# Performance work log

Measured on AMD Instinct MI355X. Metric: run time of the kernel, lower is better.

The kernel has to match this reference:

```python
import jax, jax.numpy as jnp
import numpy as np

BETA = 0.99      # rootfind_module beta
TOL = 1e-3       # torch loop: while V(fx*a) - t > 0.001
MAX_ITER = 50    # safety cap (torch loop is uncapped but converges)


def _fhat(x, W1, b1, W2, b2):
    # x: (B,1,D) -> (B,1,D)
    h = jnp.tanh(x @ W1 + b1)
    return h @ W2 + b2


def _V_sample(z, Wv1, Wv2):
    # z: (1,D) -> scalar Lyapunov value
    h = jnp.tanh(z @ Wv1)
    y = h @ Wv2
    return jnp.sum(y * y) + 0.01 * jnp.sum(z * z)


def _V(z, Wv1, Wv2):
    # z: (B,1,D) -> (B,1,1)
    h = jnp.tanh(z @ Wv1)
    y = h @ Wv2
    v = jnp.sum(y * y, axis=(-2, -1)) + 0.01 * jnp.sum(z * z, axis=(-2, -1))
    return v[:, None, None]


def _newton_step(fhatx, target, alpha, Wv1, Wv2):
    # newton_iter.forward: F = alpha - (V(fhatx*alpha) - target) / dV/dalpha
    z = fhatx * alpha                                  # (B,1,D)
    Vz = _V(z, Wv1, Wv2)                               # (B,1,1)
    gradV = jax.vmap(jax.grad(_V_sample), in_axes=(0, None, None))(z, Wv1, Wv2)
    dV_da = jnp.sum(gradV * fhatx, axis=(-2, -1))[:, None, None]
    return alpha - (Vz - target) / dV_da


def _rootfind(fhatx, target, Wv1, Wv2):
    # batched, masked replacement of torch per-sample Python while loops
    B = fhatx.shape[0]
    alpha0 = jnp.ones((B, 1, 1), fhatx.dtype)

    def cond(carry):
        i, alpha = carry
        resid = _V(fhatx * alpha, Wv1, Wv2) - target
        return jnp.logical_and(i < MAX_ITER, jnp.any(resid > TOL))

    def body(carry):
        i, alpha = carry
        resid = _V(fhatx * alpha, Wv1, Wv2) - target
        new_alpha = _newton_step(fhatx, target, alpha, Wv1, Wv2)
        alpha = jnp.where(resid > TOL, new_alpha, alpha)  # only unconverged samples move
        return (i + 1, alpha)

    _, alpha = jax.lax.while_loop(cond, body, (jnp.int32(0), alpha0))
    return alpha


def setup_inputs() -> dict:
    key = jax.random.key(0)
    ks = jax.random.split(key, 5)
    B, D, H, HV, VO = 8192, 512, 2048, 512, 256
    s = 0.02
    return {
        "x": jax.random.normal(ks[0], (B, 1, D), jnp.float32),
        "W1": jax.random.normal(ks[1], (D, H), jnp.float32) * s,
        "b1": jnp.zeros((H,), jnp.float32),
        "W2": jax.random.normal(ks[2], (H, D), jnp.float32) * s,
        "b2": jnp.zeros((D,), jnp.float32),
        "Wv1": jax.random.normal(ks[3], (D, HV), jnp.float32) * s,
        "Wv2": jax.random.normal(ks[4], (HV, VO), jnp.float32) * s,
    }


def reference(x, W1, b1, W2, b2, Wv1, Wv2):
    fhatx = _fhat(x, W1, b1, W2, b2)        # (B,1,D)
    target = BETA * _V(x, Wv1, Wv2)         # (B,1,1)
    alpha = _rootfind(fhatx, target, Wv1, Wv2)
    return fhatx * alpha                    # x_root, (B,1,D)
```

## Files before the change

kernel.cpp:

```cpp
#include <hip/hip_runtime.h>
#include <hip/hip_bf16.h>
#include <stdint.h>
#include <stddef.h>

typedef __bf16 bf16_t;
typedef __bf16 bf16x8 __attribute__((ext_vector_type(8)));
typedef __bf16 bf16x4 __attribute__((ext_vector_type(4)));
typedef float  f32x4  __attribute__((ext_vector_type(4)));

#define NB 8192
#define ND 512
#define NH 2048
#define NHV 512
#define NVO 256
#define RF_TOL 1e-3f
#define NEWTON_MAX 16

typedef const __attribute__((address_space(1))) void gvoid_t;
typedef __attribute__((address_space(3))) void lvoid_t;

__device__ __forceinline__ void gload_lds16(const void* g, void* l) {
  __builtin_amdgcn_global_load_lds((gvoid_t*)g, (lvoid_t*)l, 16, 0, 0);
}

__device__ __forceinline__ float fast_tanhf(float x) {
  x = fminf(fmaxf(x, -15.0f), 15.0f);
  float e = __expf(2.0f * x);
  return (e - 1.0f) * __builtin_amdgcn_rcpf(e + 1.0f);
}

struct GJob {
  const bf16_t* A;
  const bf16_t* Bt;
  const float*  bias;
  bf16_t* Cbf;
  float*  Cf;
  int N, K, nbx, tanh_act;
};

__global__ __launch_bounds__(512, 2)
void gemm256_kernel(GJob j0, GJob j1)
{
  __shared__ bf16_t As[2 * 256 * 64];
  __shared__ bf16_t Bs[2 * 256 * 64];

  int f = (int)blockIdx.y * (int)gridDim.x + (int)blockIdx.x;
  const int nwg = (int)gridDim.x * (int)gridDim.y;
  f = (f & 7) * (nwg >> 3) + (f >> 3);
  const int bx0 = f % (int)gridDim.x, by = f / (int)gridDim.x;

  const bool first = bx0 < j0.nbx;
  const GJob jb = first ? j0 : j1;
  const int bx = bx0 - (first ? 0 : j0.nbx);
  const int K = jb.K, N = jb.N;

  const int t = threadIdx.x, lane = t & 63, w = t >> 6;
  const int wm = w >> 2, wn = w & 3;
  const int la = lane & 15, lg = lane >> 4;
  const size_t m0 = (size_t)by * 256, n0 = (size_t)bx * 256;

  int soff[4];
#pragma unroll
  for (int j = 0; j < 4; ++j) {
    const int off = t * 16 + j * 8192;
    const int r = off >> 7, c = off & 127;
    soff[j] = r * K + ((c ^ ((r & 7) << 4)) >> 1);
  }
  const bf16_t* Ab = jb.A + m0 * K;
  const bf16_t* Bb = jb.Bt + n0 * K;

  const int swz = (la & 7) << 4;
  const int sw0 = (lg * 16) ^ swz;
  const int sw1 = (64 + lg * 16) ^ swz;
  const int abase = (wm * 128 + la) * 128;
  const int bbase = (wn * 64 + la) * 128;

  f32x4 acc[8][4] = {};
  const int NT = K >> 6;

#pragma unroll
  for (int j = 0; j < 4; ++j) gload_lds16(Ab + soff[j], (char*)As + (t * 16 + j * 8192));
#pragma unroll
  for (int j = 0; j < 4; ++j) gload_lds16(Bb + soff[j], (char*)Bs + (t * 16 + j * 8192));
#pragma unroll
  for (int j = 0; j < 4; ++j) gload_lds16(Ab + soff[j] + 64, (char*)As + 32768 + (t * 16 + j * 8192));
#pragma unroll
  for (int j = 0; j < 4; ++j) gload_lds16(Bb + soff[j] + 64, (char*)Bs + 32768 + (t * 16 + j * 8192));

  for (int ts = 0; ts < NT; ++ts) {
    if (ts < NT - 1) asm volatile("s_waitcnt vmcnt(8)" ::: "memory");
    else             asm volatile("s_waitcnt vmcnt(0)" ::: "memory");
    __builtin_amdgcn_s_barrier();
    asm volatile("" ::: "memory");

    const char* pa = (const char*)As + (ts & 1) * 32768;
    const char* pb = (const char*)Bs + (ts & 1) * 32768;
    bf16x8 afr[8][2], bfr[4][2];
#pragma unroll
    for (int i = 0; i < 8; ++i) {
      afr[i][0] = *(const bf16x8*)(pa + abase + i * 2048 + sw0);
      afr[i][1] = *(const bf16x8*)(pa + abase + i * 2048 + sw1);
    }
#pragma unroll
    for (int j = 0; j < 4; ++j) {
      bfr[j][0] = *(const bf16x8*)(pb + bbase + j * 2048 + sw0);
      bfr[j][1] = *(const bf16x8*)(pb + bbase + j * 2048 + sw1);
    }
    asm volatile("s_waitcnt lgkmcnt(0)" ::: "memory");
    __builtin_amdgcn_s_barrier();
    asm volatile("" ::: "memory");

    if (ts + 2 < NT) {
      const int k0 = (ts + 2) << 6;
      char* da = (char*)As + (ts & 1) * 32768;
      char* db = (char*)Bs + (ts & 1) * 32768;
#pragma unroll
      for (int j = 0; j < 4; ++j) gload_lds16(Ab + soff[j] + k0, da + (t * 16 + j * 8192));
#pragma unroll
      for (int j = 0; j < 4; ++j) gload_lds16(Bb + soff[j] + k0, db + (t * 16 + j * 8192));
    }

#pragma unroll
    for (int ks = 0; ks < 2; ++ks)
#pragma unroll
      for (int i = 0; i < 8; ++i)
#pragma unroll
        for (int j = 0; j < 4; ++j)
          acc[i][j] = __builtin_amdgcn_mfma_f32_16x16x32_bf16(afr[i][ks], bfr[j][ks], acc[i][j], 0, 0, 0);
  }

#pragma unroll
  for (int i = 0; i < 8; ++i) {
#pragma unroll
    for (int j = 0; j < 4; ++j) {
      const size_t col = n0 + wn * 64 + j * 16 + la;
      const float bv = jb.bias ? jb.bias[col] : 0.0f;
#pragma unroll
      for (int r = 0; r < 4; ++r) {
        const size_t row = m0 + wm * 128 + i * 16 + lg * 4 + r;
        float v = acc[i][j][r] + bv;
        if (jb.tanh_act) v = fast_tanhf(v);
        if (jb.Cbf) jb.Cbf[row * N + col] = (bf16_t)v;
        if (jb.Cf)  jb.Cf [row * N + col] = v;
      }
    }
  }
}

template<int BM>
__global__ __launch_bounds__(256, 4)
void gemm_kernel(GJob j0, GJob j1)
{
  constexpr int MI = BM / 32;
  __shared__ bf16_t As[BM * 64];
  __shared__ bf16_t Bs[128 * 64];
  const bool first = (int)blockIdx.x < j0.nbx;
  const GJob jb = first ? j0 : j1;
  const int bx = (int)blockIdx.x - (first ? 0 : j0.nbx);
  const int K = jb.K, N = jb.N;

  const int t = threadIdx.x, lane = t & 63, w = t >> 6;
  const int wm = w >> 1, wn = w & 1;
  const int la = lane & 15, lg = lane >> 4;
  const size_t m0 = (size_t)blockIdx.y * BM, n0 = (size_t)bx * 128;

  size_t soffA[MI], soffB[4]; int doff[4];
#pragma unroll
  for (int j = 0; j < 4; ++j) {
    const int off = t * 16 + j * 4096;
    const int r = off >> 7, c = off & 127;
    const size_t so = (size_t)r * K + ((c ^ ((r & 7) << 4)) >> 1);
    if (j < MI) soffA[j] = so;
    soffB[j] = so;
    doff[j] = off;
  }
  const bf16_t* Ab = jb.A + m0 * K;
  const bf16_t* Bb = jb.Bt + n0 * K;

  int abyte[MI][2], bbyte[4][2];
#pragma unroll
  for (int ks = 0; ks < 2; ++ks) {
#pragma unroll
    for (int i = 0; i < MI; ++i) {
      const int ra = wm * (BM / 2) + i * 16 + la;
      abyte[i][ks] = ra * 128 + ((ks * 64 + lg * 16) ^ ((ra & 7) << 4));
    }
#pragma unroll
    for (int j = 0; j < 4; ++j) {
      const int rb = wn * 64 + j * 16 + la;
      bbyte[j][ks] = rb * 128 + ((ks * 64 + lg * 16) ^ ((rb & 7) << 4));
    }
  }

  f32x4 acc[MI][4] = {};
  const int nsteps = K >> 6;

  for (int ts = 0; ts < nsteps; ++ts) {
    const int k0 = ts << 6;
#pragma unroll
    for (int j = 0; j < MI; ++j)
      gload_lds16(Ab + soffA[j] + k0, (char*)As + doff[j]);
#pragma unroll
    for (int j = 0; j < 4; ++j)
      gload_lds16(Bb + soffB[j] + k0, (char*)Bs + doff[j]);
    __syncthreads();

    bf16x8 afr[MI][2], bfr[4][2];
#pragma unroll
    for (int ks = 0; ks < 2; ++ks) {
#pragma unroll
      for (int i = 0; i < MI; ++i)
        afr[i][ks] = *(const bf16x8*)((const char*)As + abyte[i][ks]);
#pragma unroll
      for (int j = 0; j < 4; ++j)
        bfr[j][ks] = *(const bf16x8*)((const char*)Bs + bbyte[j][ks]);
    }
#pragma unroll
    for (int ks = 0; ks < 2; ++ks)
#pragma unroll
      for (int i = 0; i < MI; ++i)
#pragma unroll
        for (int j = 0; j < 4; ++j)
          acc[i][j] = __builtin_amdgcn_mfma_f32_16x16x32_bf16(afr[i][ks], bfr[j][ks], acc[i][j], 0, 0, 0);
    __syncthreads();
  }

#pragma unroll
  for (int i = 0; i < MI; ++i) {
#pragma unroll
    for (int j = 0; j < 4; ++j) {
      const size_t col = n0 + wn * 64 + j * 16 + la;
      const float bv = jb.bias ? jb.bias[col] : 0.0f;
#pragma unroll
      for (int r = 0; r < 4; ++r) {
        const size_t row = m0 + wm * (BM / 2) + i * 16 + lg * 4 + r;
        float v = acc[i][j][r] + bv;
        if (jb.tanh_act) v = fast_tanhf(v);
        if (jb.Cbf) jb.Cbf[row * N + col] = (bf16_t)v;
        if (jb.Cf)  jb.Cf [row * N + col] = v;
      }
    }
  }
}

__device__ __forceinline__ void tr_body(const float* __restrict__ src, bf16_t* __restrict__ dst,
                                        int R, int C, int bidx, float (*tile)[33]) {
  const int tilesx = C >> 5;
  const int bi = (bidx / tilesx) << 5, bj = (bidx % tilesx) << 5;
  const int t = threadIdx.x, tx = t & 31, ty = t >> 5;
#pragma unroll
  for (int r = ty; r < 32; r += 8)
    tile[r][tx] = src[(size_t)(bi + r) * C + (bj + tx)];
  __syncthreads();
#pragma unroll
  for (int r = ty; r < 32; r += 8)
    dst[(size_t)(bj + r) * R + (bi + tx)] = (bf16_t)tile[tx][r];
}

__global__ void prep_kernel(const float* __restrict__ x, bf16_t* __restrict__ xbf, float* __restrict__ xsq,
                            const float* __restrict__ W1, bf16_t* __restrict__ w1t,
                            const float* __restrict__ W2, bf16_t* __restrict__ w2t,
                            const float* __restrict__ Wv1, bf16_t* __restrict__ wv1t,
                            const float* __restrict__ Wv2, bf16_t* __restrict__ wv2t)
{
  __shared__ float tile[32][33];
  const int b = blockIdx.x;
  if (b < 1024)      tr_body(W1, w1t, 512, 2048, b, tile);
  else if (b < 2048) tr_body(W2, w2t, 2048, 512, b - 1024, tile);
  else if (b < 2304) tr_body(Wv1, wv1t, 512, 512, b - 2048, tile);
  else if (b < 2432) tr_body(Wv2, wv2t, 512, 256, b - 2304, tile);
  else {
    const int t = threadIdx.x;
    const int row = (b - 2432) * 4 + (t >> 6), l = t & 63;
    const float4* sr = (const float4*)(x + (size_t)row * ND);
    bf16x4* dw = (bf16x4*)(xbf + (size_t)row * ND);
    float s = 0.0f;
#pragma unroll
    for (int c = l; c < ND / 4; c += 64) {
      float4 v = sr[c];
      s = fmaf(v.x, v.x, fmaf(v.y, v.y, fmaf(v.z, v.z, fmaf(v.w, v.w, s))));
      bf16x4 o;
      o[0] = (bf16_t)v.x; o[1] = (bf16_t)v.y; o[2] = (bf16_t)v.z; o[3] = (bf16_t)v.w;
      dw[c] = o;
    }
#pragma unroll
    for (int m = 32; m; m >>= 1) s += __shfl_xor(s, m);
    if (l == 0) xsq[row] = s;
  }
}

__global__ void post_kernel(const bf16_t* __restrict__ fbf, const float* __restrict__ yx,
                            const float* __restrict__ xsq,
                            float* __restrict__ fsq, float* __restrict__ tgt)
{
  const int b = blockIdx.x, t = threadIdx.x, l = t & 63;
  if (t < 64) {
    bf16x8 v = *(const bf16x8*)(fbf + (size_t)b * ND + l * 8);
    float s = 0.0f;
#pragma unroll
    for (int q = 0; q < 8; ++q) { float f = (float)v[q]; s = fmaf(f, f, s); }
#pragma unroll
    for (int m = 32; m; m >>= 1) s += __shfl_xor(s, m);
    if (l == 0) fsq[b] = s;
  } else {
    float4 v = ((const float4*)(yx + (size_t)b * NVO))[l];
    float s = fmaf(v.x, v.x, fmaf(v.y, v.y, fmaf(v.z, v.z, v.w * v.w)));
#pragma unroll
    for (int m = 32; m; m >>= 1) s += __shfl_xor(s, m);
    if (l == 0) tgt[b] = 0.99f * (s + 0.01f * xsq[b]);
  }
}

__global__ __launch_bounds__(512, 2)
void newton_kernel(const bf16_t* __restrict__ u0, const bf16_t* __restrict__ Wv2t,
                   const float* __restrict__ fsq, const float* __restrict__ tgt,
                   const float* __restrict__ fhat, float* __restrict__ out)
{
  __shared__ alignas(16) bf16_t hs[32 * 512];
  __shared__ alignas(16) bf16_t es[32 * 512];
  __shared__ float red[8][32][2];
  __shared__ float alpha_s[32], fsq_s[32], tgt_s[32];
  __shared__ int notdone_s;

  const int t = threadIdx.x, lane = t & 63, w = t >> 6;
  const int la = lane & 15, lg = lane >> 4;
  const int s_base = blockIdx.x * 32;
  const int arow = lane & 31, ahi = lane >> 5;

  bf16x8 bfr[2][16];
#pragma unroll
  for (int nt = 0; nt < 2; ++nt) {
    const bf16_t* bp = Wv2t + (size_t)(w * 32 + nt * 16 + la) * NHV + lg * 8;
#pragma unroll
    for (int k = 0; k < 16; ++k)
      bfr[nt][k] = *(const bf16x8*)(bp + k * 32);
  }

  bf16x8 ureg[4];
#pragma unroll
  for (int i = 0; i < 4; ++i)
    ureg[i] = *(const bf16x8*)(u0 + (size_t)(s_base + arow) * NHV + (w * 8 + ahi * 4 + i) * 8);

  if (t < 32) {
    alpha_s[t] = 1.0f;
    fsq_s[t] = fsq[s_base + t];
    tgt_s[t] = tgt[s_base + t];
  }
  __syncthreads();

  for (int it = 0; it < NEWTON_MAX; ++it) {
    {
      const float c2 = 2.0f * alpha_s[arow];
#pragma unroll
      for (int i = 0; i < 4; ++i) {
        const int k8 = w * 8 + ahi * 4 + i;
        const int byte = (arow << 10) + ((k8 ^ (arow & 7)) << 4);
        bf16x8 uv = ureg[i], hf, ef;
#pragma unroll
        for (int q = 0; q < 8; ++q) {
          float u = (float)uv[q];
          float e = __expf(c2 * u);
          float h = (e - 1.0f) * __builtin_amdgcn_rcpf(e + 1.0f);
          hf[q] = (bf16_t)h;
          ef[q] = (bf16_t)(u * (1.0f - h * h));
        }
        *(bf16x8*)((char*)hs + byte) = hf;
        *(bf16x8*)((char*)es + byte) = ef;
      }
    }
    __syncthreads();

    f32x4 accy[2][2] = {};
    f32x4 accw[2][2] = {};
#pragma unroll
    for (int k = 0; k < 16; ++k) {
#pragma unroll
      for (int mt = 0; mt < 2; ++mt) {
        const int row = mt * 16 + la;
        const int byte = (row << 10) + (((k * 4 + lg) ^ (row & 7)) << 4);
        bf16x8 hf = *(const bf16x8*)((const char*)hs + byte);
        bf16x8 ef = *(const bf16x8*)((const char*)es + byte);
#pragma unroll
        for (int nt = 0; nt < 2; ++nt) {
          accy[mt][nt] = __builtin_amdgcn_mfma_f32_16x16x32_bf16(hf, bfr[nt][k], accy[mt][nt], 0, 0, 0);
          accw[mt][nt] = __builtin_amdgcn_mfma_f32_16x16x32_bf16(ef, bfr[nt][k], accw[mt][nt], 0, 0, 0);
        }
      }
    }

#pragma unroll
    for (int mt = 0; mt < 2; ++mt) {
#pragma unroll
      for (int r = 0; r < 4; ++r) {
        float sy = 0.0f, sw = 0.0f;
#pragma unroll
        for (int nt = 0; nt < 2; ++nt) {
          float yv = accy[mt][nt][r], wv = accw[mt][nt][r];
          sy = fmaf(yv, yv, sy);
          sw = fmaf(yv, wv, sw);
        }
        sy += __shfl_xor(sy, 1); sw += __shfl_xor(sw, 1);
        sy += __shfl_xor(sy, 2); sw += __shfl_xor(sw, 2);
        sy += __shfl_xor(sy, 4); sw += __shfl_xor(sw, 4);
        sy += __shfl_xor(sy, 8); sw += __shfl_xor(sw, 8);
        if (la == 0) {
          red[w][mt * 16 + lg * 4 + r][0] = sy;
          red[w][mt * 16 + lg * 4 + r][1] = sw;
        }
      }
    }
    __syncthreads();
    if (t < 32) {
      float SY = 0.0f, SW = 0.0f;
#pragma unroll
      for (int w8 = 0; w8 < 8; ++w8) {
        SY += red[w8][t][0];
        SW += red[w8][t][1];
      }
      float a = alpha_s[t];
      const float fs = fsq_s[t];
      const float V = SY + 0.01f * a * a * fs;
      const float dV = 2.0f * SW + 0.02f * a * fs;
      const float resid = V - tgt_s[t];
      const bool go = resid > RF_TOL;
      if (go) alpha_s[t] = a - resid / dV;
      const int nd = __any(go);
      if (t == 0) notdone_s = nd;
    }
    __syncthreads();
    if (!notdone_s) break;
  }

  {
    const int r = t >> 4;
    const int c4 = t & 15;
    const float a = alpha_s[r];
    const size_t rb = (size_t)(s_base + r) * ND;
    const float4* sp = (const float4*)(fhat + rb);
    float4* dp = (float4*)(out + rb);
#pragma unroll
    for (int jj = 0; jj < 8; ++jj) {
      float4 v = sp[c4 + jj * 16];
      v.x *= a; v.y *= a; v.z *= a; v.w *= a;
      dp[c4 + jj * 16] = v;
    }
  }
}

extern "C" void kernel_launch(void* const* d_in, const int* in_sizes, int n_in,
                              void* d_out, int out_size, void* d_ws, size_t ws_size,
                              hipStream_t stream)
{
  (void)in_sizes; (void)n_in; (void)out_size; (void)ws_size;
  const float* x   = (const float*)d_in[0];
  const float* W1  = (const float*)d_in[1];
  const float* b1  = (const float*)d_in[2];
  const float* W2  = (const float*)d_in[3];
  const float* b2  = (const float*)d_in[4];
  const float* Wv1 = (const float*)d_in[5];
  const float* Wv2 = (const float*)d_in[6];
  float* out = (float*)d_out;

  char* ws = (char*)d_ws;
  size_t off = 0;
  auto alloc = [&](size_t n) { char* p = ws + off; off += (n + 255) & ~(size_t)255; return p; };

  bf16_t* xbf  = (bf16_t*)alloc((size_t)NB * ND * 2);
  bf16_t* w1t  = (bf16_t*)alloc((size_t)NH * ND * 2);
  bf16_t* w2t  = (bf16_t*)alloc((size_t)ND * NH * 2);
  bf16_t* wv1t = (bf16_t*)alloc((size_t)NHV * ND * 2);
  bf16_t* wv2t = (bf16_t*)alloc((size_t)NVO * NHV * 2);
  bf16_t* h1   = (bf16_t*)alloc((size_t)NB * NH * 2);
  float*  fhat = (float*)alloc((size_t)NB * ND * 4);
  bf16_t* fbf  = (bf16_t*)alloc((size_t)NB * ND * 2);
  bf16_t* hx   = (bf16_t*)alloc((size_t)NB * NHV * 2);
  float*  yx   = (float*)alloc((size_t)NB * NVO * 4);
  bf16_t* u0bf = (bf16_t*)alloc((size_t)NB * NHV * 2);
  float*  xsq  = (float*)alloc((size_t)NB * 4);
  float*  fsq  = (float*)alloc((size_t)NB * 4);
  float*  tgt  = (float*)alloc((size_t)NB * 4);

  prep_kernel<<<4480, 256, 0, stream>>>(x, xbf, xsq, W1, w1t, W2, w2t, Wv1, wv1t, Wv2, wv2t);

  GJob jh1 { xbf, w1t,  b1,      h1,  nullptr, NH,  ND, NH  / 256, 1 };
  GJob jhx { xbf, wv1t, nullptr, hx,  nullptr, NHV, ND, NHV / 256, 1 };
  gemm256_kernel<<<dim3(NH / 256 + NHV / 256, NB / 256), 512, 0, stream>>>(jh1, jhx);

  GJob jf  { h1,  w2t,  b2,      fbf, fhat,    ND,  NH, ND  / 128, 0 };
  GJob jy  { hx,  wv2t, nullptr, nullptr, yx,  NVO, NHV, NVO / 128, 0 };
  gemm_kernel<64><<<dim3(ND / 128 + NVO / 128, NB / 64), 256, 0, stream>>>(jf, jy);

  post_kernel<<<NB, 128, 0, stream>>>(fbf, yx, xsq, fsq, tgt);

  GJob ju  { fbf, wv1t, nullptr, u0bf, nullptr, NHV, ND, NHV / 128, 0 };
  gemm_kernel<64><<<dim3(NHV / 128, NB / 64), 256, 0, stream>>>(ju, ju);

  newton_kernel<<<NB / 32, 512, 0, stream>>>(u0bf, wv2t, fsq, tgt, fhat, out);
}
```

Baseline: 137.2 us.

## Replace 256x256 first-layer GEMM with triple-buffered 256x128 split-phase kernel

The first GEMM (x@W1 and x@Wv1 fused) now uses 256x128 tiles with a three-stage LDS ring instead of two-stage double buffering. Each k-step is split into two half-tiles of MFMAs, with A and B prefetches interleaved between them and s_setprio raised around the MFMA blocks. The aim is to overlap global loads and LDS reads with matrix math and to double the grid size for better CU fill. In exchange each tile reuses less data, and occupancy falls to one workgroup per CU because of the larger LDS footprint.

Measured after the change: 132.9 us. 3.2% less time.

```diff
diff --git a/kernel.cpp b/kernel.cpp
--- a/kernel.cpp
+++ b/kernel.cpp
@@ -38,11 +38,10 @@
   int N, K, nbx, tanh_act;
 };
 
-__global__ __launch_bounds__(512, 2)
-void gemm256_kernel(GJob j0, GJob j1)
+__global__ __launch_bounds__(512, 1)
+void gemm_tri_kernel(GJob j0, GJob j1)
 {
-  __shared__ bf16_t As[2 * 256 * 64];
-  __shared__ bf16_t Bs[2 * 256 * 64];
+  __shared__ bf16_t lds3[3 * 24576];
 
   int f = (int)blockIdx.y * (int)gridDim.x + (int)blockIdx.x;
   const int nwg = (int)gridDim.x * (int)gridDim.y;
@@ -57,83 +56,108 @@
   const int t = threadIdx.x, lane = t & 63, w = t >> 6;
   const int wm = w >> 2, wn = w & 3;
   const int la = lane & 15, lg = lane >> 4;
-  const size_t m0 = (size_t)by * 256, n0 = (size_t)bx * 256;
-
-  int soff[4];
-#pragma unroll
-  for (int j = 0; j < 4; ++j) {
-    const int off = t * 16 + j * 8192;
-    const int r = off >> 7, c = off & 127;
-    soff[j] = r * K + ((c ^ ((r & 7) << 4)) >> 1);
-  }
+  const size_t m0 = (size_t)by * 256, n0 = (size_t)bx * 128;
+
   const bf16_t* Ab = jb.A + m0 * K;
   const bf16_t* Bb = jb.Bt + n0 * K;
+  char* ldsB = (char*)lds3;
+
+  const int r0 = t >> 3;
+  const int swc = (((t & 7) * 16) ^ ((r0 & 7) << 4)) >> 1;
+  const int sA0 = r0 * K + swc;
 
   const int swz = (la & 7) << 4;
   const int sw0 = (lg * 16) ^ swz;
   const int sw1 = (64 + lg * 16) ^ swz;
-  const int abase = (wm * 128 + la) * 128;
-  const int bbase = (wn * 64 + la) * 128;
-
-  f32x4 acc[8][4] = {};
+  const int abase = wm * 16384 + la * 128;
+  const int bbase = 32768 + (wn * 32 + la) * 128;
+
+  f32x4 acc[8][2] = {};
   const int NT = K >> 6;
 
-#pragma unroll
-  for (int j = 0; j < 4; ++j) gload_lds16(Ab + soff[j], (char*)As + (t * 16 + j * 8192));
-#pragma unroll
-  for (int j = 0; j < 4; ++j) gload_lds16(Bb + soff[j], (char*)Bs + (t * 16 + j * 8192));
-#pragma unroll
-  for (int j = 0; j < 4; ++j) gload_lds16(Ab + soff[j] + 64, (char*)As + 32768 + (t * 16 + j * 8192));
-#pragma unroll
-  for (int j = 0; j < 4; ++j) gload_lds16(Bb + soff[j] + 64, (char*)Bs + 32768 + (t * 16 + j * 8192));
-
-  for (int ts = 0; ts < NT; ++ts) {
-    if (ts < NT - 1) asm volatile("s_waitcnt vmcnt(8)" ::: "memory");
-    else             asm volatile("s_waitcnt vmcnt(0)" ::: "memory");
+#define STAGE_A(kt_) do { \
+    char* dA = ldsB + ((kt_) % 3) * 49152; \
+    const int ko = (kt_) << 6; \
+    gload_lds16(Ab + sA0 + ko,               dA + t * 16); \
+    gload_lds16(Ab + sA0 + 64 * K + ko,      dA + t * 16 + 8192); \
+    gload_lds16(Ab + 128 * K + sA0 + ko,     dA + 16384 + t * 16); \
+    gload_lds16(Ab + 192 * K + sA0 + ko,     dA + 16384 + t * 16 + 8192); \
+  } while (0)
+#define STAGE_B(kt_) do { \
+    char* dB = ldsB + ((kt_) % 3) * 49152 + 32768; \
+    const int ko = (kt_) << 6; \
+    gload_lds16(Bb + sA0 + ko,               dB + t * 16); \
+    gload_lds16(Bb + sA0 + 64 * K + ko,      dB + t * 16 + 8192); \
+  } while (0)
+
+  STAGE_A(0); STAGE_B(0);
+  STAGE_A(1); STAGE_B(1);
+  asm volatile("s_waitcnt vmcnt(6)" ::: "memory");
+  __builtin_amdgcn_s_barrier();
+  asm volatile("" ::: "memory");
+
+  for (int kt = 0; kt < NT; ++kt) {
+    const char* pb = ldsB + (kt % 3) * 49152;
+    const bool st = (kt + 2 < NT);
+
+    bf16x8 bfr[2][2], afr[4][2];
+#pragma unroll
+    for (int j = 0; j < 2; ++j) {
+      bfr[j][0] = *(const bf16x8*)(pb + bbase + j * 2048 + sw0);
+      bfr[j][1] = *(const bf16x8*)(pb + bbase + j * 2048 + sw1);
+    }
+#pragma unroll
+    for (int i = 0; i < 4; ++i) {
+      afr[i][0] = *(const bf16x8*)(pb + abase + i * 2048 + sw0);
+      afr[i][1] = *(const bf16x8*)(pb + abase + i * 2048 + sw1);
+    }
+    if (st) STAGE_A(kt + 2);
+    asm volatile("s_waitcnt lgkmcnt(8)" ::: "memory");
+    __builtin_amdgcn_s_barrier();
+    asm volatile("s_waitcnt lgkmcnt(0)" ::: "memory");
+    __builtin_amdgcn_s_setprio(1);
+#pragma unroll
+    for (int ks = 0; ks < 2; ++ks)
+#pragma unroll
+      for (int i = 0; i < 4; ++i)
+#pragma unroll
+        for (int j = 0; j < 2; ++j)
+          acc[i][j] = __builtin_amdgcn_mfma_f32_16x16x32_bf16(afr[i][ks], bfr[j][ks], acc[i][j], 0, 0, 0);
+    __builtin_amdgcn_s_setprio(0);
     __builtin_amdgcn_s_barrier();
     asm volatile("" ::: "memory");
 
-    const char* pa = (const char*)As + (ts & 1) * 32768;
-    const char* pb = (const char*)Bs + (ts & 1) * 32768;
-    bf16x8 afr[8][2], bfr[4][2];
-#pragma unroll
-    for (int i = 0; i < 8; ++i) {
-      afr[i][0] = *(const bf16x8*)(pa + abase + i * 2048 + sw0);
-      afr[i][1] = *(const bf16x8*)(pa + abase + i * 2048 + sw1);
-    }
-#pragma unroll
-    for (int j = 0; j < 4; ++j) {
-      bfr[j][0] = *(const bf16x8*)(pb + bbase + j * 2048 + sw0);
-      bfr[j][1] = *(const bf16x8*)(pb + bbase + j * 2048 + sw1);
-    }
+    bf16x8 af2[4][2];
+#pragma unroll
+    for (int i = 0; i < 4; ++i) {
+      af2[i][0] = *(const bf16x8*)(pb + abase + (i + 4) * 2048 + sw0);
+      af2[i][1] = *(const bf16x8*)(pb + abase + (i + 4) * 2048 + sw1);
+    }
+    if (st) STAGE_B(kt + 2);
+    if (st)                asm volatile("s_waitcnt vmcnt(6)" ::: "memory");
+    else if (kt + 1 < NT)  asm volatile("s_waitcnt vmcnt(0)" ::: "memory");
+    __builtin_amdgcn_s_barrier();
     asm volatile("s_waitcnt lgkmcnt(0)" ::: "memory");
+    __builtin_amdgcn_s_setprio(1);
+#pragma unroll
+    for (int ks = 0; ks < 2; ++ks)
+#pragma unroll
+      for (int i = 0; i < 4; ++i)
+#pragma unroll
+        for (int j = 0; j < 2; ++j)
+          acc[i + 4][j] = __builtin_amdgcn_mfma_f32_16x16x32_bf16(af2[i][ks], bfr[j][ks], acc[i + 4][j], 0, 0, 0);
+    __builtin_amdgcn_s_setprio(0);
     __builtin_amdgcn_s_barrier();
     asm volatile("" ::: "memory");
-
-    if (ts + 2 < NT) {
-      const int k0 = (ts + 2) << 6;
-      char* da = (char*)As + (ts & 1) * 32768;
-      char* db = (char*)Bs + (ts & 1) * 32768;
-#pragma unroll
-      for (int j = 0; j < 4; ++j) gload_lds16(Ab + soff[j] + k0, da + (t * 16 + j * 8192));
-#pragma unroll
-      for (int j = 0; j < 4; ++j) gload_lds16(Bb + soff[j] + k0, db + (t * 16 + j * 8192));
-    }
-
-#pragma unroll
-    for (int ks = 0; ks < 2; ++ks)
-#pragma unroll
-      for (int i = 0; i < 8; ++i)
-#pragma unroll
-        for (int j = 0; j < 4; ++j)
-          acc[i][j] = __builtin_amdgcn_mfma_f32_16x16x32_bf16(afr[i][ks], bfr[j][ks], acc[i][j], 0, 0, 0);
-  }
+  }
+#undef STAGE_A
+#undef STAGE_B
 
 #pragma unroll
   for (int i = 0; i < 8; ++i) {
 #pragma unroll
-    for (int j = 0; j < 4; ++j) {
-      const size_t col = n0 + wn * 64 + j * 16 + la;
+    for (int j = 0; j < 2; ++j) {
+      const size_t col = n0 + wn * 32 + j * 16 + la;
       const float bv = jb.bias ? jb.bias[col] : 0.0f;
 #pragma unroll
       for (int r = 0; r < 4; ++r) {
@@ -482,9 +506,9 @@
 
   prep_kernel<<<4480, 256, 0, stream>>>(x, xbf, xsq, W1, w1t, W2, w2t, Wv1, wv1t, Wv2, wv2t);
 
-  GJob jh1 { xbf, w1t,  b1,      h1,  nullptr, NH,  ND, NH  / 256, 1 };
-  GJob jhx { xbf, wv1t, nullptr, hx,  nullptr, NHV, ND, NHV / 256, 1 };
-  gemm256_kernel<<<dim3(NH / 256 + NHV / 256, NB / 256), 512, 0, stream>>>(jh1, jhx);
+  GJob jh1 { xbf, w1t,  b1,      h1,  nullptr, NH,  ND, NH  / 128, 1 };
+  GJob jhx { xbf, wv1t, nullptr, hx,  nullptr, NHV, ND, NHV / 128, 1 };
+  gemm_tri_kernel<<<dim3(NH / 128 + NHV / 128, NB / 256), 512, 0, stream>>>(jh1, jhx);
 
   GJob jf  { h1,  w2t,  b2,      fbf, fhat,    ND,  NH, ND  / 128, 0 };
   GJob jy  { hx,  wv2t, nullptr, nullptr, yx,  NVO, NHV, NVO / 128, 0 };
```
